# Performance work log

Measured on AMD Instinct MI355X. Metric: run time of the kernel, lower is better.

Reference implementation:

```python
import jax, jax.numpy as jnp
import numpy as np


def _hadamard(n: int) -> np.ndarray:
    # Sylvester construction; n must be a power of 2 (asserted in the torch source).
    H = np.array([[1.0]], dtype=np.float32)
    while H.shape[0] < n:
        H = np.block([[H, H], [H, -H]])
    return (H * (n ** -0.5)).astype(np.float32)


def _rotate_activation(x):
    # hadamard_transform(x, scale=D**-0.5) over the last dim; bf16 in/out like the CUDA kernel.
    D = x.shape[-1]
    H = jnp.asarray(_hadamard(D))
    return (x.astype(jnp.float32) @ H).astype(x.dtype)


def _cu_seqlen_kv_bounds(seq_lens, num_ctx_tokens):
    # Vectorized equivalent of compute_cu_seqlen_kv_bounds_nocache (repeat_interleave -> searchsorted).
    offsets = jnp.concatenate([jnp.zeros(1, jnp.int32), jnp.cumsum(seq_lens).astype(jnp.int32)])
    pos = jnp.arange(num_ctx_tokens, dtype=jnp.int32)
    batch_ids = jnp.searchsorted(offsets, pos, side='right').astype(jnp.int32) - 1
    ks = offsets[batch_ids]                 # start of this token's sequence in packed KV
    ke = ks + (pos - ks) + 1                # causal: local_position + 1 past the start
    return ks, ke


def setup_inputs() -> dict:
    key = jax.random.key(0)
    k1, k2, k3 = jax.random.split(key, 3)
    T, H, D = 2048, 16, 128
    q = jax.random.normal(k1, (T, H, D), dtype=jnp.bfloat16)
    k = jax.random.normal(k2, (T, D), dtype=jnp.bfloat16)
    weights = jax.random.uniform(k3, (T, H), dtype=jnp.float32) * (H ** -0.5)
    seq_lens = jnp.array([1024, 1024], dtype=jnp.int32)
    return {"q": q, "k": k, "weights": weights, "seq_lens": seq_lens, "index_topk": 256}


def reference(q, k, weights, seq_lens, index_topk):
    T = q.shape[0]
    # Hadamard-rotate q and k (lightning indexer activation rotation).
    qr = _rotate_activation(q).astype(jnp.float32)   # [T, H, D]
    kr = _rotate_activation(k).astype(jnp.float32)   # [T, D]
    # Index score: I[t, s] = sum_h w[t, h] * relu(q[t, h] . k[s])
    logits = jnp.einsum('thd,sd->ths', qr, kr)       # [T, H, T]
    scores = jnp.einsum('ths,th->ts', jax.nn.relu(logits), weights)  # [T, T]
    # Causal ragged-batch KV window per token.
    ks, ke = _cu_seqlen_kv_bounds(seq_lens, T)
    pos = jnp.arange(T, dtype=jnp.int32)
    valid = (pos[None, :] >= ks[:, None]) & (pos[None, :] < ke[:, None])
    NEG = jnp.float32(-1e30)
    masked = jnp.where(valid, scores, NEG)
    topk_vals, topk_idx = jax.lax.top_k(masked, index_topk)  # [T, topk]
    return topk_vals, topk_idx
```

## Files before the change

### kernel.cpp

```cpp
#include <hip/hip_runtime.h>
#include <hip/hip_bf16.h>
#include <stdint.h>

typedef __attribute__((ext_vector_type(8))) short short8;
typedef __attribute__((ext_vector_type(4))) float float4_t;

#define DDIM 128
#define SORTN 256
#define LROW 136
#define SCAP 1088
#define NCHT 17

__device__ inline unsigned short f32_to_bf16_rne(float f) {
    uint32_t u = __float_as_uint(f);
    return (unsigned short)((u + 0x7FFFu + ((u >> 16) & 1u)) >> 16);
}
__device__ inline float bf16_to_f32(unsigned short h) {
    return __uint_as_float(((uint32_t)h) << 16);
}
__device__ inline int ks_of(const int* seq_lens, int n_seq, int t) {
    int off = 0, r = 0;
    for (int i = 0; i < n_seq; ++i) {
        int nx = off + seq_lens[i];
        if (t < nx) { r = off; break; }
        off = nx;
    }
    return r;
}

__global__ __launch_bounds__(256) void rotate_k_kernel(
        const unsigned short* __restrict__ k, unsigned short* __restrict__ kr, int T) {
    int row = blockIdx.x * 16 + (threadIdx.x >> 4);
    if (row >= T) return;
    int l16 = threadIdx.x & 15;
    short8 in = *(const short8*)(k + (size_t)row * DDIM + 8 * l16);
    float f[8];
    #pragma unroll
    for (int j = 0; j < 8; ++j) f[j] = bf16_to_f32((unsigned short)in[j]);
    #pragma unroll
    for (int b = 1; b <= 4; b <<= 1)
        #pragma unroll
        for (int j = 0; j < 8; ++j)
            if (!(j & b)) { float a = f[j], c = f[j | b]; f[j] = a + c; f[j | b] = a - c; }
    #pragma unroll
    for (int m = 1; m <= 8; m <<= 1) {
        bool hi = (l16 & m) != 0;
        #pragma unroll
        for (int j = 0; j < 8; ++j) {
            float o = __shfl_xor(f[j], m, 64);
            f[j] = hi ? (o - f[j]) : (f[j] + o);
        }
    }
    const float sc = 0.08838834764831845f;
    short8 out;
    #pragma unroll
    for (int j = 0; j < 8; ++j) out[j] = (short)f32_to_bf16_rne(f[j] * sc);
    *(short8*)(kr + (size_t)row * DDIM + 8 * l16) = out;
}

__global__ __launch_bounds__(256, 3) void fused_kernel(
        const unsigned short* __restrict__ q,
        const unsigned short* __restrict__ kr,
        const float* __restrict__ w,
        const int* __restrict__ seq_lens, int n_seq,
        float* __restrict__ out_vals, float* __restrict__ out_idx,
        int T, int H, int K, int Tt) {
    __shared__ __align__(16) unsigned short bL[128 * LROW];
    __shared__ __align__(16) float scw[4][SCAP];

    const int tid  = threadIdx.x;
    const int wv   = tid >> 6, lane = tid & 63;
    const int col  = lane & 15, kgrp = lane >> 4;
    const int srow = tid >> 4, sseg = tid & 15;

    const int m     = blockIdx.x;
    const int ttile = (m & 1) ? (Tt - 1 - (m >> 1)) : (m >> 1);
    const int tt0   = ttile * 4;
    const int t_w   = tt0 + wv;
    const bool wvalid = (t_w < T);
    const int t_c  = wvalid ? t_w : T - 1;
    const int ks_w = ks_of(seq_lens, n_seq, t_c);
    const int ke_w = t_c + 1;
    const int n    = ke_w - ks_w;

    const int bks   = ks_of(seq_lens, n_seq, tt0);
    const int bke   = (tt0 + 4 < T) ? (tt0 + 4) : T;
    const int ntile = (bke - bks + 127) >> 7;

    float f[4][8];
    const unsigned short* qrow = q + ((size_t)t_c * H + col) * DDIM + kgrp * 8;
    #pragma unroll
    for (int kk = 0; kk < 4; ++kk) {
        short8 v = *(const short8*)(qrow + kk * 32);
        #pragma unroll
        for (int j = 0; j < 8; ++j) f[kk][j] = bf16_to_f32((unsigned short)v[j]);
    }
    #pragma unroll
    for (int b = 1; b <= 4; b <<= 1)
        #pragma unroll
        for (int kk = 0; kk < 4; ++kk)
            #pragma unroll
            for (int j = 0; j < 8; ++j)
                if (!(j & b)) { float a = f[kk][j], c = f[kk][j | b];
                                f[kk][j] = a + c; f[kk][j | b] = a - c; }
    #pragma unroll
    for (int kk = 0; kk < 4; ++kk)
        #pragma unroll
        for (int j = 0; j < 8; ++j) {
            float o = __shfl_xor(f[kk][j], 16, 64);
            f[kk][j] = (kgrp & 1) ? (o - f[kk][j]) : (f[kk][j] + o);
        }
    #pragma unroll
    for (int kk = 0; kk < 4; ++kk)
        #pragma unroll
        for (int j = 0; j < 8; ++j) {
            float o = __shfl_xor(f[kk][j], 32, 64);
            f[kk][j] = (kgrp & 2) ? (o - f[kk][j]) : (f[kk][j] + o);
        }
    #pragma unroll
    for (int j = 0; j < 8; ++j) {
        { float a = f[0][j], c = f[1][j]; f[0][j] = a + c; f[1][j] = a - c; }
        { float a = f[2][j], c = f[3][j]; f[2][j] = a + c; f[3][j] = a - c; }
        { float a = f[0][j], c = f[2][j]; f[0][j] = a + c; f[2][j] = a - c; }
        { float a = f[1][j], c = f[3][j]; f[1][j] = a + c; f[3][j] = a - c; }
    }
    short8 afrag[4];
    const float scl = 0.08838834764831845f;
    #pragma unroll
    for (int kk = 0; kk < 4; ++kk)
        #pragma unroll
        for (int j = 0; j < 8; ++j)
            afrag[kk][j] = (short)f32_to_bf16_rne(f[kk][j] * scl);

    float w4[4];
    #pragma unroll
    for (int r = 0; r < 4; ++r) w4[r] = w[(size_t)t_c * H + kgrp * 4 + r];

    for (int c = 0; c < ntile; ++c) {
        const int kv0 = bks + c * 128;
        #pragma unroll
        for (int it = 0; it < 8; ++it) {
            int gs = kv0 + srow + 16 * it; if (gs > T - 1) gs = T - 1;
            *(short8*)&bL[(srow + 16 * it) * LROW + sseg * 8] =
                *(const short8*)(kr + (size_t)gs * DDIM + sseg * 8);
        }
        __syncthreads();
        #pragma unroll
        for (int nt = 0; nt < 8; ++nt) {
            float4_t acc = {0.f, 0.f, 0.f, 0.f};
            #pragma unroll
            for (int kk = 0; kk < 4; ++kk) {
                short8 bf = *(const short8*)&bL[(nt * 16 + col) * LROW + kgrp * 8 + kk * 32];
                acc = __builtin_amdgcn_mfma_f32_16x16x32_bf16(afrag[kk], bf, acc, 0, 0, 0);
            }
            float p = 0.f;
            #pragma unroll
            for (int r = 0; r < 4; ++r) {
                float v = acc[r];
                v = v > 0.f ? v : 0.f;
                p += w4[r] * v;
            }
            p += __shfl_xor(p, 16, 64);
            p += __shfl_xor(p, 32, 64);
            int s = kv0 + nt * 16 + col;
            if (wvalid && lane < 16 && s >= ks_w && s <= t_w)
                scw[wv][s - ks_w] = p;
        }
        __syncthreads();
    }

    const int nch = (n + 63) >> 6;
    uint32_t ukey[NCHT];
    #pragma unroll
    for (int c = 0; c < NCHT; ++c) {
        if (c < nch) {
            int i = c * 64 + lane;
            ukey[c] = (wvalid && i < n) ? __float_as_uint(scw[wv][i]) : 0u;
        } else ukey[c] = 0u;
    }
    __syncthreads();
    unsigned long long* candw = (unsigned long long*)&scw[wv][0];

    if (!wvalid) return;

    const int Keff = (n < K) ? n : K;
    uint32_t ustar = 0;
    int ttake = K;
    if (n > K) {
        uint32_t lo = 0, hi = 0x80000000u;
        for (int it = 0; it < 31; ++it) {
            uint32_t mid = (lo + hi) >> 1;
            int lc = 0;
            #pragma unroll
            for (int c = 0; c < NCHT; ++c)
                if (c < nch) lc += (ukey[c] >= mid) ? 1 : 0;
            #pragma unroll
            for (int off = 1; off <= 32; off <<= 1)
                lc += __shfl_xor(lc, off, 64);
            if (lc >= K) lo = mid; else hi = mid;
        }
        ustar = lo;
        int lg = 0;
        #pragma unroll
        for (int c = 0; c < NCHT; ++c)
            if (c < nch) lg += (ukey[c] > ustar) ? 1 : 0;
        #pragma unroll
        for (int off = 1; off <= 32; off <<= 1)
            lg += __shfl_xor(lg, off, 64);
        ttake = K - lg;
    }

    {
        const unsigned long long ltm = (1ull << lane) - 1ull;
        int base = 0, tieBase = 0;
        const bool selAll = (n <= K);
        #pragma unroll
        for (int c = 0; c < NCHT; ++c) {
            if (c < nch) {
                int i = c * 64 + lane;
                bool inb = (i < n);
                uint32_t u = ukey[c];
                bool isGt  = inb && (selAll || u > ustar);
                bool isTie = inb && !selAll && (u == ustar);
                unsigned long long mt = __ballot(isTie);
                int tr = tieBase + (int)__popcll(mt & ltm);
                bool take = isGt || (isTie && tr < ttake);
                unsigned long long mk = __ballot(take);
                if (take) {
                    int pos = base + (int)__popcll(mk & ltm);
                    int s = ks_w + i;
                    if (pos < SORTN)
                        candw[pos] = ((((unsigned long long)u << 11) |
                                       (unsigned long long)(T - 1 - s)) + 1ull);
                }
                base    += (int)__popcll(mk);
                tieBase += (int)__popcll(mt);
            }
        }
        for (int i = Keff + lane; i < SORTN; i += 64) candw[i] = 0ull;
    }

    unsigned long long kreg[4];
    #pragma unroll
    for (int r = 0; r < 4; ++r) kreg[r] = candw[4 * lane + r];

    #define CX(a, b, dsc) { unsigned long long _mx = (a) > (b) ? (a) : (b); \
                            unsigned long long _mn = (a) > (b) ? (b) : (a); \
                            (a) = (dsc) ? _mx : _mn; (b) = (dsc) ? _mn : _mx; }
    #pragma unroll
    for (int size = 2; size <= SORTN; size <<= 1) {
        #pragma unroll
        for (int stride = SORTN >> 1; stride >= 4; stride >>= 1) {
            if (stride > (size >> 1)) continue;
            int lmask = stride >> 2;
            #pragma unroll
            for (int r = 0; r < 4; ++r) {
                int e = 4 * lane + r;
                unsigned long long other = __shfl_xor(kreg[r], lmask, 64);
                bool desc = ((e & size) == 0);
                bool iAmLow = ((e & stride) == 0);
                bool keepMax = (iAmLow == desc);
                kreg[r] = keepMax ? (kreg[r] > other ? kreg[r] : other)
                                  : (kreg[r] < other ? kreg[r] : other);
            }
        }
        if (size >= 4) {
            bool d = (((4 * lane) & size) == 0);
            CX(kreg[0], kreg[2], d);
            CX(kreg[1], kreg[3], d);
            CX(kreg[0], kreg[1], d);
            CX(kreg[2], kreg[3], d);
        } else {
            CX(kreg[0], kreg[1], true);
            CX(kreg[2], kreg[3], false);
        }
    }
    #undef CX

    if (4 * lane < K) {
        float4_t v4, i4;
        #pragma unroll
        for (int r = 0; r < 4; ++r) {
            int e = 4 * lane + r;
            unsigned long long key = kreg[r];
            float v; int idx;
            if (key != 0ull) {
                unsigned long long km1 = key - 1ull;
                v = __uint_as_float((uint32_t)(km1 >> 11));
                idx = T - 1 - (int)(km1 & 0x7FFull);
            } else {
                int pidx = e - Keff;
                idx = (pidx < ks_w) ? pidx : (ke_w + (pidx - ks_w));
                v = -1e30f;
            }
            v4[r] = v; i4[r] = (float)idx;
        }
        *(float4_t*)(out_vals + (size_t)t_w * K + 4 * lane) = v4;
        *(float4_t*)(out_idx  + (size_t)t_w * K + 4 * lane) = i4;
    }
}

extern "C" void kernel_launch(void* const* d_in, const int* in_sizes, int n_in,
                              void* d_out, int out_size, void* d_ws, size_t ws_size,
                              hipStream_t stream) {
    const unsigned short* q = (const unsigned short*)d_in[0];
    const unsigned short* k = (const unsigned short*)d_in[1];
    const float* w          = (const float*)d_in[2];
    const int* seq_lens     = (const int*)d_in[3];
    const int n_seq = in_sizes[3];
    const int T = in_sizes[1] / DDIM;
    const int H = in_sizes[2] / T;
    const int K = out_size / (2 * T);

    unsigned short* kr = (unsigned short*)d_ws;
    float* out_vals = (float*)d_out;
    float* out_idx  = out_vals + (size_t)T * K;

    rotate_k_kernel<<<dim3((T + 15) / 16), dim3(256), 0, stream>>>(k, kr, T);
    const int Tt = (T + 3) / 4;
    fused_kernel<<<dim3(Tt), dim3(256), 0, stream>>>(
        q, kr, w, seq_lens, n_seq, out_vals, out_idx, T, H, K, Tt);
}
```

Before: 113.5 us.

## Split score MMA across two wave halves, prefetch K tiles, use DPP reductions

Blocks grow to 512 threads, with two waves per token each computing half of the 16-column score tiles per KV chunk. The next KV tile is prefetched into registers while the current one is being computed, and it is written to shared memory after a barrier. The binary-search count reductions switch from shuffles to DPP row operations plus readlane. The upper-half waves exit before top-k selection, so they sit idle during that phase, and register pressure rises from the prefetch buffers under the new launch bounds.

```diff
diff --git a/kernel.cpp b/kernel.cpp
--- a/kernel.cpp
+++ b/kernel.cpp
@@ -26,6 +26,16 @@
         off = nx;
     }
     return r;
+}
+
+__device__ inline int wave_reduce_add_dpp(int x) {
+    x += __builtin_amdgcn_update_dpp(0, x, 0x111, 0xF, 0xF, true);
+    x += __builtin_amdgcn_update_dpp(0, x, 0x112, 0xF, 0xF, true);
+    x += __builtin_amdgcn_update_dpp(0, x, 0x114, 0xF, 0xF, true);
+    x += __builtin_amdgcn_update_dpp(0, x, 0x118, 0xF, 0xF, true);
+    x += __builtin_amdgcn_update_dpp(0, x, 0x142, 0xA, 0xF, true);
+    x += __builtin_amdgcn_update_dpp(0, x, 0x143, 0xC, 0xF, true);
+    return __builtin_amdgcn_readlane(x, 63);
 }
 
 __global__ __launch_bounds__(256) void rotate_k_kernel(
@@ -58,7 +68,7 @@
     *(short8*)(kr + (size_t)row * DDIM + 8 * l16) = out;
 }
 
-__global__ __launch_bounds__(256, 3) void fused_kernel(
+__global__ __launch_bounds__(512, 4) void fused_kernel(
         const unsigned short* __restrict__ q,
         const unsigned short* __restrict__ kr,
         const float* __restrict__ w,
@@ -70,13 +80,14 @@
 
     const int tid  = threadIdx.x;
     const int wv   = tid >> 6, lane = tid & 63;
+    const int tok  = wv & 3, half = wv >> 2;
     const int col  = lane & 15, kgrp = lane >> 4;
     const int srow = tid >> 4, sseg = tid & 15;
 
     const int m     = blockIdx.x;
     const int ttile = (m & 1) ? (Tt - 1 - (m >> 1)) : (m >> 1);
     const int tt0   = ttile * 4;
-    const int t_w   = tt0 + wv;
+    const int t_w   = tt0 + tok;
     const bool wvalid = (t_w < T);
     const int t_c  = wvalid ? t_w : T - 1;
     const int ks_w = ks_of(seq_lens, n_seq, t_c);
@@ -87,6 +98,16 @@
     const int bke   = (tt0 + 4 < T) ? (tt0 + 4) : T;
     const int ntile = (bke - bks + 127) >> 7;
 
+    short8 pre[4];
+    {
+        int kv0 = bks;
+        #pragma unroll
+        for (int it = 0; it < 4; ++it) {
+            int gs = kv0 + srow + 32 * it; if (gs > T - 1) gs = T - 1;
+            pre[it] = *(const short8*)(kr + (size_t)gs * DDIM + sseg * 8);
+        }
+    }
+
     float f[4][8];
     const unsigned short* qrow = q + ((size_t)t_c * H + col) * DDIM + kgrp * 8;
     #pragma unroll
@@ -136,17 +157,24 @@
     #pragma unroll
     for (int r = 0; r < 4; ++r) w4[r] = w[(size_t)t_c * H + kgrp * 4 + r];
 
+    #pragma unroll
+    for (int it = 0; it < 4; ++it)
+        *(short8*)&bL[(srow + 32 * it) * LROW + sseg * 8] = pre[it];
+    __syncthreads();
+
     for (int c = 0; c < ntile; ++c) {
         const int kv0 = bks + c * 128;
-        #pragma unroll
-        for (int it = 0; it < 8; ++it) {
-            int gs = kv0 + srow + 16 * it; if (gs > T - 1) gs = T - 1;
-            *(short8*)&bL[(srow + 16 * it) * LROW + sseg * 8] =
-                *(const short8*)(kr + (size_t)gs * DDIM + sseg * 8);
-        }
-        __syncthreads();
-        #pragma unroll
-        for (int nt = 0; nt < 8; ++nt) {
+        if (c + 1 < ntile) {
+            int kvn = kv0 + 128;
+            #pragma unroll
+            for (int it = 0; it < 4; ++it) {
+                int gs = kvn + srow + 32 * it; if (gs > T - 1) gs = T - 1;
+                pre[it] = *(const short8*)(kr + (size_t)gs * DDIM + sseg * 8);
+            }
+        }
+        #pragma unroll
+        for (int nth = 0; nth < 4; ++nth) {
+            const int nt = half * 4 + nth;
             float4_t acc = {0.f, 0.f, 0.f, 0.f};
             #pragma unroll
             for (int kk = 0; kk < 4; ++kk) {
@@ -164,10 +192,18 @@
             p += __shfl_xor(p, 32, 64);
             int s = kv0 + nt * 16 + col;
             if (wvalid && lane < 16 && s >= ks_w && s <= t_w)
-                scw[wv][s - ks_w] = p;
+                scw[tok][s - ks_w] = p;
         }
         __syncthreads();
-    }
+        if (c + 1 < ntile) {
+            #pragma unroll
+            for (int it = 0; it < 4; ++it)
+                *(short8*)&bL[(srow + 32 * it) * LROW + sseg * 8] = pre[it];
+            __syncthreads();
+        }
+    }
+
+    if (half == 1 || !wvalid) return;
 
     const int nch = (n + 63) >> 6;
     uint32_t ukey[NCHT];
@@ -175,13 +211,10 @@
     for (int c = 0; c < NCHT; ++c) {
         if (c < nch) {
             int i = c * 64 + lane;
-            ukey[c] = (wvalid && i < n) ? __float_as_uint(scw[wv][i]) : 0u;
+            ukey[c] = (i < n) ? __float_as_uint(scw[tok][i]) : 0u;
         } else ukey[c] = 0u;
     }
-    __syncthreads();
-    unsigned long long* candw = (unsigned long long*)&scw[wv][0];
-
-    if (!wvalid) return;
+    unsigned long long* candw = (unsigned long long*)&scw[tok][0];
 
     const int Keff = (n < K) ? n : K;
     uint32_t ustar = 0;
@@ -194,20 +227,15 @@
             #pragma unroll
             for (int c = 0; c < NCHT; ++c)
                 if (c < nch) lc += (ukey[c] >= mid) ? 1 : 0;
-            #pragma unroll
-            for (int off = 1; off <= 32; off <<= 1)
-                lc += __shfl_xor(lc, off, 64);
-            if (lc >= K) lo = mid; else hi = mid;
+            int total = wave_reduce_add_dpp(lc);
+            if (total >= K) lo = mid; else hi = mid;
         }
         ustar = lo;
         int lg = 0;
         #pragma unroll
         for (int c = 0; c < NCHT; ++c)
             if (c < nch) lg += (ukey[c] > ustar) ? 1 : 0;
-        #pragma unroll
-        for (int off = 1; off <= 32; off <<= 1)
-            lg += __shfl_xor(lg, off, 64);
-        ttake = K - lg;
+        ttake = K - wave_reduce_add_dpp(lg);
     }
 
     {
@@ -318,6 +346,6 @@
 
     rotate_k_kernel<<<dim3((T + 15) / 16), dim3(256), 0, stream>>>(k, kr, T);
     const int Tt = (T + 3) / 4;
-    fused_kernel<<<dim3(Tt), dim3(256), 0, stream>>>(
+    fused_kernel<<<dim3(Tt), dim3(512), 0, stream>>>(
         q, kr, w, seq_lens, n_seq, out_vals, out_idx, T, H, K, Tt);
 }
```

Measured after the change: 105.4 us. 1.08x faster.
